# Optimization experiments

Hardware: AMD Instinct MI355X
Metric: run time of the kernel (lower is better)

The kernel has to match this reference:

```python
import jax, jax.numpy as jnp
import numpy as np
import math

N_HEADS = 32
N_KV_HEADS = 8
HEAD_DIM = 64
ROPE_BASE = 10000.0


def _rope_cos_sin(L, dtype):
    # inv_freq: [head_dim/2]
    inv_freq = 1.0 / (ROPE_BASE ** (jnp.arange(0, HEAD_DIM, 2, dtype=jnp.float32) / HEAD_DIM))
    t = jnp.arange(L, dtype=jnp.float32)
    freqs = jnp.outer(t, inv_freq)            # [L, head_dim/2]
    emb = jnp.concatenate([freqs, freqs], -1)  # [L, head_dim]
    return jnp.cos(emb).astype(dtype), jnp.sin(emb).astype(dtype)


def _rotate_half(x):
    x1, x2 = jnp.split(x, 2, axis=-1)
    return jnp.concatenate([-x2, x1], axis=-1)


def setup_inputs() -> dict:
    key = jax.random.key(0)
    ks = jax.random.split(key, 5)
    B, L, D = 2, 2048, 2048
    s = 0.02
    return {
        "x": jax.random.normal(ks[0], (B, L, D), jnp.float32),
        "Wq": jax.random.normal(ks[1], (D, N_HEADS * HEAD_DIM), jnp.float32) * s,
        "Wk": jax.random.normal(ks[2], (D, N_KV_HEADS * HEAD_DIM), jnp.float32) * s,
        "Wv": jax.random.normal(ks[3], (D, N_KV_HEADS * HEAD_DIM), jnp.float32) * s,
        "Wo": jax.random.normal(ks[4], (N_HEADS * HEAD_DIM, D), jnp.float32) * s,
    }


def reference(x, Wq, Wk, Wv, Wo):
    B, L, D = x.shape
    G = N_HEADS // N_KV_HEADS
    # QKV projections -> [B, H, L, hd]
    q = (x @ Wq).reshape(B, L, N_HEADS, HEAD_DIM).transpose(0, 2, 1, 3)
    k = (x @ Wk).reshape(B, L, N_KV_HEADS, HEAD_DIM).transpose(0, 2, 1, 3)
    v = (x @ Wv).reshape(B, L, N_KV_HEADS, HEAD_DIM).transpose(0, 2, 1, 3)
    # RoPE
    cos, sin = _rope_cos_sin(L, x.dtype)  # [L, hd]
    cos = cos[None, None]
    sin = sin[None, None]
    q = q * cos + _rotate_half(q) * sin
    k = k * cos + _rotate_half(k) * sin
    # GQA expand kv heads (repeat_interleave along head dim)
    k = jnp.repeat(k, G, axis=1)
    v = jnp.repeat(v, G, axis=1)
    # Causal SDPA
    scale = 1.0 / math.sqrt(HEAD_DIM)
    scores = jnp.einsum('bhqd,bhkd->bhqk', q, k) * scale  # [B,H,L,L]
    causal = jnp.tril(jnp.ones((L, L), bool))
    scores = jnp.where(causal[None, None], scores, jnp.finfo(scores.dtype).min)
    probs = jax.nn.softmax(scores, axis=-1)
    out = jnp.einsum('bhqk,bhkd->bhqd', probs, v)  # [B,H,L,hd]
    out = out.transpose(0, 2, 1, 3).reshape(B, L, N_HEADS * HEAD_DIM)
    return out @ Wo
```

## Files before the change

kernel.cpp:

```cpp
#include <hip/hip_runtime.h>
#include <hip/hip_bf16.h>
#include <stdint.h>

typedef __bf16 bf16_t;
typedef bf16_t bf16x2 __attribute__((ext_vector_type(2)));
typedef bf16_t bf16x4 __attribute__((ext_vector_type(4)));
typedef bf16_t bf16x8 __attribute__((ext_vector_type(8)));
typedef float f32x4 __attribute__((ext_vector_type(4)));
typedef float f32x16 __attribute__((ext_vector_type(16)));

#define NH 32
#define NKV 8
#define HD 64
#define LSEQ 2048
#define DMODEL 2048
#define BATCH 2

#define QSCALE 0.18033688011112042f
#define FIXED_M 12.0f

__device__ __forceinline__ void gl_lds16(const void* g, void* l) {
  __builtin_amdgcn_global_load_lds(
      (__attribute__((address_space(1))) char*)(uintptr_t)g,
      (__attribute__((address_space(3))) char*)(uintptr_t)l, 16, 0, 0);
}

__device__ __forceinline__ unsigned pack2(float a, float b) {
  bf16x2 t;
  t[0] = (bf16_t)a;
  t[1] = (bf16_t)b;
  return __builtin_bit_cast(unsigned, t);
}

__device__ __forceinline__ void transpose_tile32(
    const float* __restrict__ W, bf16_t* __restrict__ WT, int K, int N,
    int bi, float* tile ) {
  const int n32 = N >> 5;
  const int nb = (bi & (n32 - 1)) * 32, kb = (bi / n32) * 32;
  const int tx = threadIdx.x & 31, ty = threadIdx.x >> 5;
#pragma unroll
  for (int i = 0; i < 32; i += 8)
    tile[(ty + i) * 33 + tx] = W[(size_t)(kb + ty + i) * N + nb + tx];
  __syncthreads();
#pragma unroll
  for (int i = 0; i < 32; i += 8)
    WT[(size_t)(nb + ty + i) * K + kb + tx] = (bf16_t)tile[tx * 33 + ty + i];
}

__global__ __launch_bounds__(256) void prep_all(
    const float* __restrict__ x, const float* __restrict__ Wq,
    const float* __restrict__ Wk, const float* __restrict__ Wv,
    const float* __restrict__ Wo, bf16_t* __restrict__ xb,
    bf16_t* __restrict__ wqkvT, bf16_t* __restrict__ wot,
    float* __restrict__ cosT, float* __restrict__ sinT) {
  __shared__ float tile[32 * 33];
  const int bx = blockIdx.x;
  if (bx < 8192) {
    const int i = bx * 256 + threadIdx.x;
    const float4 v = ((const float4*)x)[i];
    bf16x4 o;
    o[0] = (bf16_t)v.x; o[1] = (bf16_t)v.y; o[2] = (bf16_t)v.z; o[3] = (bf16_t)v.w;
    ((bf16x4*)xb)[i] = o;
  } else if (bx < 12288) {
    transpose_tile32(Wq, wqkvT, 2048, 2048, bx - 8192, tile);
  } else if (bx < 13312) {
    transpose_tile32(Wk, wqkvT + (size_t)2048 * 2048, 2048, 512, bx - 12288, tile);
  } else if (bx < 14336) {
    transpose_tile32(Wv, wqkvT + (size_t)2560 * 2048, 2048, 512, bx - 13312, tile);
  } else if (bx < 18432) {
    transpose_tile32(Wo, wot, 2048, 2048, bx - 14336, tile);
  } else {
    const int t = (bx - 18432) * 256 + threadIdx.x;
    const int l = t >> 5, i = t & 31;
    const float inv = powf(10000.0f, -(float)i / 32.0f);
    const float ang = (float)l * inv;
    float s, c;
    sincosf(ang, &s, &c);
    cosT[t] = c;
    sinT[t] = s;
  }
}

template <int EPI>
__global__ __launch_bounds__(256, 3) void gemm128(
    const bf16_t* __restrict__ A, const bf16_t* __restrict__ BT,
    float* __restrict__ Cf, bf16_t* __restrict__ Qo, bf16_t* __restrict__ Ko,
    bf16_t* __restrict__ Vo, int M, int N, int K,
    const float* __restrict__ cosT, const float* __restrict__ sinT, int nx) {
  __shared__ bf16_t Al[128 * 64];
  __shared__ bf16_t Bl[128 * 64];
  const int tid = threadIdx.x, lane = tid & 63, w = tid >> 6;
  const int wm = w >> 1, wn = w & 1;
  const int r15 = lane & 15, g = lane >> 4;
  const int nwg = (int)gridDim.x;
  const int sid = ((int)blockIdx.x & 7) * (nwg >> 3) + ((int)blockIdx.x >> 3);
  const int m0 = (sid / nx) * 128, n0 = (sid % nx) * 128;
  f32x4 acc[4][4] = {};

  for (int kt = 0; kt < K; kt += 64) {
#pragma unroll
    for (int i = 0; i < 4; ++i) {
      const int c = i * 256 + tid;
      const int row = c >> 3, cc = c & 7;
      const int sc = (cc ^ (row & 7)) * 8;
      gl_lds16(A + (size_t)(m0 + row) * K + kt + sc, Al + c * 8);
      gl_lds16(BT + (size_t)(n0 + row) * K + kt + sc, Bl + c * 8);
    }
    __syncthreads();
#pragma unroll
    for (int kk = 0; kk < 2; ++kk) {
      bf16x8 af[4], bfr[4];
#pragma unroll
      for (int mi = 0; mi < 4; ++mi) {
        const int r = wm * 64 + mi * 16 + r15;
        af[mi] = *(const bf16x8*)((const char*)Al + r * 128 +
                                  (((kk * 4 + g) ^ (r & 7)) << 4));
      }
#pragma unroll
      for (int ni = 0; ni < 4; ++ni) {
        const int r = wn * 64 + ni * 16 + r15;
        bfr[ni] = *(const bf16x8*)((const char*)Bl + r * 128 +
                                   (((kk * 4 + g) ^ (r & 7)) << 4));
      }
#pragma unroll
      for (int mi = 0; mi < 4; ++mi)
#pragma unroll
        for (int ni = 0; ni < 4; ++ni)
          acc[mi][ni] = __builtin_amdgcn_mfma_f32_16x16x32_bf16(
              af[mi], bfr[ni], acc[mi][ni], 0, 0, 0);
    }
    __syncthreads();
  }

  if constexpr (EPI == 0) {
#pragma unroll
    for (int mi = 0; mi < 4; ++mi) {
      const int row = m0 + wm * 64 + mi * 16 + g * 4;
#pragma unroll
      for (int ni = 0; ni < 4; ++ni) {
        const int col = n0 + wn * 64 + ni * 16 + r15;
#pragma unroll
        for (int r = 0; r < 4; ++r)
          Cf[(size_t)(row + r) * N + col] = acc[mi][ni][r];
      }
    }
  } else {
    const int colbase = n0 + wn * 64;
    auto rope_store = [&](bf16_t* C, int NHT, int colrel, float sc) {
#pragma unroll
      for (int mi = 0; mi < 4; ++mi)
#pragma unroll
        for (int r = 0; r < 4; ++r) {
          const int rowg = m0 + wm * 64 + mi * 16 + g * 4 + r;
          const int bb = rowg >> 11, ls = rowg & (LSEQ - 1);
#pragma unroll
          for (int ni = 0; ni < 2; ++ni) {
            const int col = colrel + ni * 16 + r15;
            const int hh = col >> 6, d = col & 63;
            const float c = cosT[ls * 32 + d], s = sinT[ls * 32 + d];
            const float v0 = acc[mi][ni][r], v1 = acc[mi][ni + 2][r];
            bf16_t* dst = C + (((size_t)bb * NHT + hh) * LSEQ + ls) * HD + d;
            dst[0] = (bf16_t)((v0 * c - v1 * s) * sc);
            dst[32] = (bf16_t)((v1 * c + v0 * s) * sc);
          }
        }
    };
    if (n0 < 2048) {
      rope_store(Qo, NH, colbase, QSCALE);
    } else if (n0 < 2560) {
      rope_store(Ko, NKV, colbase - 2048, 1.0f);
    } else {
#pragma unroll
      for (int mi = 0; mi < 4; ++mi)
#pragma unroll
        for (int r = 0; r < 4; ++r) {
          const int rowg = m0 + wm * 64 + mi * 16 + g * 4 + r;
          const int bb = rowg >> 11, ls = rowg & (LSEQ - 1);
#pragma unroll
          for (int ni = 0; ni < 4; ++ni) {
            const int col = colbase - 2560 + ni * 16 + r15;
            const int hh = col >> 6, d = col & 63;
            Vo[(((size_t)bb * NKV + hh) * HD + d) * LSEQ + ls] =
                (bf16_t)acc[mi][ni][r];
          }
        }
    }
  }
}

template <int EPI, int NREP>
__global__ __launch_bounds__(512, 1) void gemm256(
    const bf16_t* __restrict__ A, const bf16_t* __restrict__ BT,
    float* __restrict__ Cf, int M, int N, int K, int nx) {
  __shared__ bf16_t Al[2][4 * 4096];
  __shared__ bf16_t Bl[2][NREP * 4096];
  const int tid = threadIdx.x, lane = tid & 63, w = tid >> 6;
  const int wm = w >> 2, wn = w & 3;
  const int r15 = lane & 15, g = lane >> 4;
  const int nwg = (int)gridDim.x;
  const int sid = ((int)blockIdx.x & 7) * (nwg >> 3) + ((int)blockIdx.x >> 3);
  const int m0 = (sid / nx) * 256, n0 = (sid % nx) * (NREP * 64);

  f32x4 acc[8][NREP] = {};

  const int NT = K >> 6;
  const int NI = NT >> 1;

  auto stage_q = [&](bf16_t* dst, const bf16_t* src, int row0, int kt) {
    const int r = tid >> 3;
    const int sc = (((tid & 7) ^ (r & 7)) << 3);
    gl_lds16(src + (size_t)(row0 + r) * K + (kt << 6) + sc, dst + tid * 8);
  };
  auto stage_step = [&](int d, int kt, int s) {
    kt = kt < NT ? kt : NT - 1;
    if (s == 0) { stage_q(&Bl[d][0], BT, n0, kt); stage_q(&Bl[d][4096], BT, n0 + 64, kt); }
    else if (s == 1) { stage_q(&Al[d][0], A, m0, kt); stage_q(&Al[d][8192], A, m0 + 128, kt); }
    else if (s == 2) { stage_q(&Al[d][4096], A, m0 + 64, kt); stage_q(&Al[d][12288], A, m0 + 192, kt); }
  };
  auto lda = [&](int d, int mi, int kk) -> bf16x8 {
    const int ar = (wm << 7) + (mi << 4) + r15;
    return *(const bf16x8*)((const char*)&Al[d][(ar >> 6) << 12] +
                            (ar & 63) * 128 + ((((kk << 2) + g) ^ (ar & 7)) << 4));
  };
  auto ldb = [&](int d, int ni, int kk) -> bf16x8 {
    const int br = wn * (NREP << 4) + (ni << 4) + r15;
    return *(const bf16x8*)((const char*)&Bl[d][(br >> 6) << 12] +
                            (br & 63) * 128 + ((((kk << 2) + g) ^ (br & 7)) << 4));
  };

  stage_step(0, 0, 0);
  stage_step(0, 0, 1);
  stage_step(0, 0, 2);
  stage_step(0, 0, 3);

  for (int i = 0; i < NI; ++i) {
#pragma unroll
    for (int hf = 0; hf < 2; ++hf) {
      const int dC = hf;
      const int dS = hf ^ 1;
      const int ktS = (i << 1) + 1 + hf;
      bf16x8 bf0[NREP][2];
#pragma unroll
      for (int q = 0; q < 4; ++q) {
        stage_step(dS, ktS, q);
        if (q == 0) asm volatile("s_waitcnt vmcnt(4)" ::: "memory");
        if (q == 2) asm volatile("s_waitcnt vmcnt(6)" ::: "memory");
        __builtin_amdgcn_s_barrier();
        asm volatile("" ::: "memory");
        if (q == 0) {
#pragma unroll
          for (int ni = 0; ni < NREP; ++ni)
#pragma unroll
            for (int kk = 0; kk < 2; ++kk) bf0[ni][kk] = ldb(dC, ni, kk);
        }
        bf16x8 af[2][2];
#pragma unroll
        for (int t2 = 0; t2 < 2; ++t2)
#pragma unroll
          for (int kk = 0; kk < 2; ++kk) af[t2][kk] = lda(dC, 2 * q + t2, kk);
        __builtin_amdgcn_s_setprio(1);
#pragma unroll
        for (int t2 = 0; t2 < 2; ++t2)
#pragma unroll
          for (int ni = 0; ni < NREP; ++ni)
#pragma unroll
            for (int kk = 0; kk < 2; ++kk)
              acc[2 * q + t2][ni] = __builtin_amdgcn_mfma_f32_16x16x32_bf16(
                  af[t2][kk], bf0[ni][kk], acc[2 * q + t2][ni], 0, 0, 0);
        __builtin_amdgcn_s_setprio(0);
        asm volatile("" ::: "memory");
        __builtin_amdgcn_s_barrier();
      }
    }
  }
  asm volatile("s_waitcnt vmcnt(0)" ::: "memory");

#pragma unroll
  for (int mi = 0; mi < 8; ++mi) {
    const int row = m0 + wm * 128 + mi * 16 + g * 4;
#pragma unroll
    for (int ni = 0; ni < NREP; ++ni) {
      const int col = n0 + wn * (NREP * 16) + ni * 16 + r15;
#pragma unroll
      for (int r = 0; r < 4; ++r)
        Cf[(size_t)(row + r) * N + col] = acc[mi][ni][r];
    }
  }
}

__global__ __launch_bounds__(512, 4) void attn_fwd(
    const bf16_t* __restrict__ Q, const bf16_t* __restrict__ Kh,
    const bf16_t* __restrict__ VTh, bf16_t* __restrict__ AO) {
  __shared__ bf16_t Kl[2][64 * 64];
  __shared__ bf16_t Vl[2][64 * 64];
  const int tid = threadIdx.x, lane = tid & 63, w = tid >> 6;
  const int col = lane & 31, hi = lane >> 5;
  const int hk = (int)blockIdx.x & 7, b = (int)blockIdx.x >> 3;
  const int a = (int)blockIdx.y & 15, k = (int)blockIdx.y >> 4;
  const int qt = k ? 31 - a : a;
  const int h = hk * 4 + (w & 3);
  const int qoff = (w >> 2) * 32;

  const bf16_t* Qb =
      Q + (((size_t)b * NH + h) * LSEQ + (size_t)qt * 64 + qoff) * HD;
  const bf16_t* Kb = Kh + ((size_t)b * NKV + hk) * LSEQ * HD;
  const bf16_t* Vb = VTh + ((size_t)b * NKV + hk) * HD * LSEQ;

  const int nt = qt + 1;

  bf16x8 ones8;
#pragma unroll
  for (int j = 0; j < 8; ++j) ones8[j] = (bf16_t)1.0f;

  auto stage = [&](int buf, int kt) {
    const int row = tid >> 3, cc = tid & 7;
    const int scol = (cc ^ (row & 7)) * 16;
    gl_lds16((const char*)Kb + (size_t)(kt * 64 + row) * 128 + scol,
             (char*)&Kl[buf][0] + tid * 16);
    gl_lds16((const char*)Vb + (size_t)row * 4096 + (size_t)kt * 128 + scol,
             (char*)&Vl[buf][0] + tid * 16);
  };

  bf16x8 qf[4];
#pragma unroll
  for (int kc = 0; kc < 4; ++kc)
    qf[kc] = *(const bf16x8*)&Qb[(size_t)col * HD + kc * 16 + hi * 8];

  f32x16 o[2] = {};
  f32x16 osum = {};

  int cur = 0;
  stage(cur, 0);
  __syncthreads();
  for (int kt = 0; kt < nt; ++kt) {
    if (kt + 1 < nt) stage(cur ^ 1, kt + 1);
    const bool diag = (kt == nt - 1);
    const char* Kcur = (const char*)&Kl[cur][0];
    const char* Vcur = (const char*)&Vl[cur][0];

    f32x16 sfrag[2] = {};
#pragma unroll
    for (int kvs = 0; kvs < 2; ++kvs) {
      if (diag && kvs * 32 > 31 + qoff) {
#pragma unroll
        for (int r = 0; r < 16; ++r) sfrag[kvs][r] = -1e30f;
        continue;
      }
      bf16x8 ak[4];
#pragma unroll
      for (int kc = 0; kc < 4; ++kc) {
        const int row = kvs * 32 + col;
        const int slot = ((kc * 2 + hi) ^ (row & 7)) * 16;
        ak[kc] = *(const bf16x8*)(Kcur + row * 128 + slot);
      }
#pragma unroll
      for (int kc = 0; kc < 4; ++kc)
        sfrag[kvs] = __builtin_amdgcn_mfma_f32_32x32x16_bf16(
            ak[kc], qf[kc], sfrag[kvs], 0, 0, 0);
    }

    if (diag) {
#pragma unroll
      for (int kvs = 0; kvs < 2; ++kvs)
#pragma unroll
        for (int r = 0; r < 16; ++r) {
          const int kvl = kvs * 32 + (r & 3) + 8 * (r >> 2) + 4 * hi;
          if (kvl > col + qoff) sfrag[kvs][r] = -1e30f;
        }
    }

    bf16x8 pf[4];
#pragma unroll
    for (int kvs = 0; kvs < 2; ++kvs)
#pragma unroll
      for (int c1 = 0; c1 < 2; ++c1) {
        float pv[8];
#pragma unroll
        for (int j = 0; j < 8; ++j)
          pv[j] = __builtin_amdgcn_exp2f(sfrag[kvs][c1 * 8 + j] - FIXED_M);
        const unsigned a01 = pack2(pv[0], pv[1]), a23 = pack2(pv[2], pv[3]);
        const unsigned b01 = pack2(pv[4], pv[5]), b23 = pack2(pv[6], pv[7]);
        const unsigned s01 = __shfl_xor(hi ? a01 : b01, 32);
        const unsigned s23 = __shfl_xor(hi ? a23 : b23, 32);
        union { unsigned u[4]; bf16x8 v; } t;
        t.u[0] = hi ? s01 : a01;
        t.u[1] = hi ? s23 : a23;
        t.u[2] = hi ? b01 : s01;
        t.u[3] = hi ? b23 : s23;
        pf[kvs * 2 + c1] = t.v;
      }

#pragma unroll
    for (int ds = 0; ds < 2; ++ds) {
      bf16x8 av[4];
#pragma unroll
      for (int kc2 = 0; kc2 < 4; ++kc2) {
        const int row = ds * 32 + col;
        const int slot = ((kc2 * 2 + hi) ^ (row & 7)) * 16;
        av[kc2] = *(const bf16x8*)(Vcur + row * 128 + slot);
      }
#pragma unroll
      for (int kc2 = 0; kc2 < 4; ++kc2) {
        if (diag && kc2 * 16 > 31 + qoff) continue;
        o[ds] = __builtin_amdgcn_mfma_f32_32x32x16_bf16(
            av[kc2], pf[kc2], o[ds], 0, 0, 0);
      }
    }
#pragma unroll
    for (int kc2 = 0; kc2 < 4; ++kc2) {
      if (diag && kc2 * 16 > 31 + qoff) continue;
      osum = __builtin_amdgcn_mfma_f32_32x32x16_bf16(
          ones8, pf[kc2], osum, 0, 0, 0);
    }

    __syncthreads();
    cur ^= 1;
  }

  const float inv = 1.0f / osum[0];
  const int q = qt * 64 + qoff + col;
#pragma unroll
  for (int ds = 0; ds < 2; ++ds)
#pragma unroll
    for (int g4 = 0; g4 < 4; ++g4) {
      bf16x4 o4;
#pragma unroll
      for (int j = 0; j < 4; ++j) o4[j] = (bf16_t)(o[ds][g4 * 4 + j] * inv);
      const int d = ds * 32 + 8 * g4 + 4 * hi;
      *(bf16x4*)&AO[((size_t)b * LSEQ + q) * DMODEL + h * HD + d] = o4;
    }
}


extern "C" void kernel_launch(void* const* d_in, const int* in_sizes, int n_in,
                              void* d_out, int out_size, void* d_ws, size_t ws_size,
                              hipStream_t stream) {
  const float* x = (const float*)d_in[0];
  const float* Wq = (const float*)d_in[1];
  const float* Wk = (const float*)d_in[2];
  const float* Wv = (const float*)d_in[3];
  const float* Wo = (const float*)d_in[4];
  char* ws = (char*)d_ws;
  size_t off = 0;
  auto alloc = [&](size_t bytes) {
    char* p = ws + off;
    off += (bytes + 255) & ~(size_t)255;
    return p;
  };
  bf16_t* xb = (bf16_t*)alloc((size_t)BATCH * LSEQ * DMODEL * 2);
  bf16_t* wqkvT = (bf16_t*)alloc((size_t)3072 * DMODEL * 2);
  bf16_t* wot = (bf16_t*)alloc((size_t)DMODEL * DMODEL * 2);
  float* cosT = (float*)alloc((size_t)LSEQ * 32 * 4);
  float* sinT = (float*)alloc((size_t)LSEQ * 32 * 4);
  bf16_t* Qh = (bf16_t*)alloc((size_t)BATCH * NH * LSEQ * HD * 2);
  bf16_t* Kh = (bf16_t*)alloc((size_t)BATCH * NKV * LSEQ * HD * 2);
  bf16_t* VTh = (bf16_t*)alloc((size_t)BATCH * NKV * HD * LSEQ * 2);
  bf16_t* AO = (bf16_t*)alloc((size_t)BATCH * LSEQ * NH * HD * 2);
  (void)ws_size; (void)in_sizes; (void)n_in; (void)out_size;

  const int M = BATCH * LSEQ;

  prep_all<<<18688, 256, 0, stream>>>(x, Wq, Wk, Wv, Wo, xb, wqkvT, wot,
                                      cosT, sinT);

  gemm128<3><<<768, 256, 0, stream>>>(
      xb, wqkvT, nullptr, Qh, Kh, VTh, M, 3072, 2048, cosT, sinT, 24);

  attn_fwd<<<dim3(16, 32), 512, 0, stream>>>(Qh, Kh, VTh, AO);

  gemm256<0, 2><<<256, 512, 0, stream>>>(
      AO, wot, (float*)d_out, M, 2048, 2048, 16);
}
```

Before: 164.8 us.

## Process two query sub-tiles per wave in attention and sum probabilities in registers

Attention blocks shrink from 8 to 4 waves. Each wave now handles all 64 query rows of its head, so every K/V fragment read from LDS is reused across two query halves. The ones-matrix MFMA that computed the softmax denominator is replaced by scalar register accumulation plus a cross-half shuffle. The trade-off is higher register pressure (two Q fragment sets, four O accumulators) and fewer waves per block to hide the staging latency.

New measurement: 175.7 us. 6.6% more time.

```diff
diff --git a/kernel.cpp b/kernel.cpp
--- a/kernel.cpp
+++ b/kernel.cpp
@@ -288,7 +288,7 @@
   }
 }
 
-__global__ __launch_bounds__(512, 4) void attn_fwd(
+__global__ __launch_bounds__(256, 2) void attn_fwd(
     const bf16_t* __restrict__ Q, const bf16_t* __restrict__ Kh,
     const bf16_t* __restrict__ VTh, bf16_t* __restrict__ AO) {
   __shared__ bf16_t Kl[2][64 * 64];
@@ -298,36 +298,37 @@
   const int hk = (int)blockIdx.x & 7, b = (int)blockIdx.x >> 3;
   const int a = (int)blockIdx.y & 15, k = (int)blockIdx.y >> 4;
   const int qt = k ? 31 - a : a;
-  const int h = hk * 4 + (w & 3);
-  const int qoff = (w >> 2) * 32;
-
-  const bf16_t* Qb =
-      Q + (((size_t)b * NH + h) * LSEQ + (size_t)qt * 64 + qoff) * HD;
+  const int h = hk * 4 + w;
+
+  const bf16_t* Qb = Q + (((size_t)b * NH + h) * LSEQ + (size_t)qt * 64) * HD;
   const bf16_t* Kb = Kh + ((size_t)b * NKV + hk) * LSEQ * HD;
   const bf16_t* Vb = VTh + ((size_t)b * NKV + hk) * HD * LSEQ;
 
   const int nt = qt + 1;
 
-  bf16x8 ones8;
-#pragma unroll
-  for (int j = 0; j < 8; ++j) ones8[j] = (bf16_t)1.0f;
-
   auto stage = [&](int buf, int kt) {
-    const int row = tid >> 3, cc = tid & 7;
-    const int scol = (cc ^ (row & 7)) * 16;
-    gl_lds16((const char*)Kb + (size_t)(kt * 64 + row) * 128 + scol,
-             (char*)&Kl[buf][0] + tid * 16);
-    gl_lds16((const char*)Vb + (size_t)row * 4096 + (size_t)kt * 128 + scol,
-             (char*)&Vl[buf][0] + tid * 16);
-  };
-
-  bf16x8 qf[4];
-#pragma unroll
-  for (int kc = 0; kc < 4; ++kc)
-    qf[kc] = *(const bf16x8*)&Qb[(size_t)col * HD + kc * 16 + hi * 8];
-
-  f32x16 o[2] = {};
-  f32x16 osum = {};
+#pragma unroll
+    for (int i = 0; i < 2; ++i) {
+      const int c = i * 256 + tid;
+      const int row = c >> 3, cc = c & 7;
+      const int scol = (cc ^ (row & 7)) * 16;
+      gl_lds16((const char*)Kb + (size_t)(kt * 64 + row) * 128 + scol,
+               (char*)&Kl[buf][0] + c * 16);
+      gl_lds16((const char*)Vb + (size_t)row * 4096 + (size_t)kt * 128 + scol,
+               (char*)&Vl[buf][0] + c * 16);
+    }
+  };
+
+  bf16x8 qf[2][4];
+#pragma unroll
+  for (int qh = 0; qh < 2; ++qh)
+#pragma unroll
+    for (int kc = 0; kc < 4; ++kc)
+      qf[qh][kc] =
+          *(const bf16x8*)&Qb[(size_t)(qh * 32 + col) * HD + kc * 16 + hi * 8];
+
+  f32x16 o[2][2] = {};
+  float lsum[2] = {0.f, 0.f};
 
   int cur = 0;
   stage(cur, 0);
@@ -338,14 +339,9 @@
     const char* Kcur = (const char*)&Kl[cur][0];
     const char* Vcur = (const char*)&Vl[cur][0];
 
-    f32x16 sfrag[2] = {};
+    bf16x8 pf[2][4];
 #pragma unroll
     for (int kvs = 0; kvs < 2; ++kvs) {
-      if (diag && kvs * 32 > 31 + qoff) {
-#pragma unroll
-        for (int r = 0; r < 16; ++r) sfrag[kvs][r] = -1e30f;
-        continue;
-      }
       bf16x8 ak[4];
 #pragma unroll
       for (int kc = 0; kc < 4; ++kc) {
@@ -354,41 +350,41 @@
         ak[kc] = *(const bf16x8*)(Kcur + row * 128 + slot);
       }
 #pragma unroll
-      for (int kc = 0; kc < 4; ++kc)
-        sfrag[kvs] = __builtin_amdgcn_mfma_f32_32x32x16_bf16(
-            ak[kc], qf[kc], sfrag[kvs], 0, 0, 0);
-    }
-
-    if (diag) {
-#pragma unroll
-      for (int kvs = 0; kvs < 2; ++kvs)
-#pragma unroll
-        for (int r = 0; r < 16; ++r) {
-          const int kvl = kvs * 32 + (r & 3) + 8 * (r >> 2) + 4 * hi;
-          if (kvl > col + qoff) sfrag[kvs][r] = -1e30f;
-        }
-    }
-
-    bf16x8 pf[4];
-#pragma unroll
-    for (int kvs = 0; kvs < 2; ++kvs)
-#pragma unroll
-      for (int c1 = 0; c1 < 2; ++c1) {
-        float pv[8];
-#pragma unroll
-        for (int j = 0; j < 8; ++j)
-          pv[j] = __builtin_amdgcn_exp2f(sfrag[kvs][c1 * 8 + j] - FIXED_M);
-        const unsigned a01 = pack2(pv[0], pv[1]), a23 = pack2(pv[2], pv[3]);
-        const unsigned b01 = pack2(pv[4], pv[5]), b23 = pack2(pv[6], pv[7]);
-        const unsigned s01 = __shfl_xor(hi ? a01 : b01, 32);
-        const unsigned s23 = __shfl_xor(hi ? a23 : b23, 32);
-        union { unsigned u[4]; bf16x8 v; } t;
-        t.u[0] = hi ? s01 : a01;
-        t.u[1] = hi ? s23 : a23;
-        t.u[2] = hi ? b01 : s01;
-        t.u[3] = hi ? b23 : s23;
-        pf[kvs * 2 + c1] = t.v;
-      }
+      for (int qh = 0; qh < 2; ++qh) {
+        if (diag && kvs == 1 && qh == 0) continue;
+        f32x16 sf = {};
+#pragma unroll
+        for (int kc = 0; kc < 4; ++kc)
+          sf = __builtin_amdgcn_mfma_f32_32x32x16_bf16(ak[kc], qf[qh][kc], sf,
+                                                       0, 0, 0);
+        if (diag && kvs == qh) {
+#pragma unroll
+          for (int r = 0; r < 16; ++r) {
+            const int kvl = (r & 3) + 8 * (r >> 2) + 4 * hi;
+            if (kvl > col) sf[r] = -1e30f;
+          }
+        }
+#pragma unroll
+        for (int c1 = 0; c1 < 2; ++c1) {
+          float pv[8];
+#pragma unroll
+          for (int j = 0; j < 8; ++j) {
+            pv[j] = __builtin_amdgcn_exp2f(sf[c1 * 8 + j] - FIXED_M);
+            lsum[qh] += pv[j];
+          }
+          const unsigned a01 = pack2(pv[0], pv[1]), a23 = pack2(pv[2], pv[3]);
+          const unsigned b01 = pack2(pv[4], pv[5]), b23 = pack2(pv[6], pv[7]);
+          const unsigned s01 = __shfl_xor(hi ? a01 : b01, 32);
+          const unsigned s23 = __shfl_xor(hi ? a23 : b23, 32);
+          union { unsigned u[4]; bf16x8 v; } t;
+          t.u[0] = hi ? s01 : a01;
+          t.u[1] = hi ? s23 : a23;
+          t.u[2] = hi ? b01 : s01;
+          t.u[3] = hi ? b23 : s23;
+          pf[qh][kvs * 2 + c1] = t.v;
+        }
+      }
+    }
 
 #pragma unroll
     for (int ds = 0; ds < 2; ++ds) {
@@ -400,35 +396,36 @@
         av[kc2] = *(const bf16x8*)(Vcur + row * 128 + slot);
       }
 #pragma unroll
-      for (int kc2 = 0; kc2 < 4; ++kc2) {
-        if (diag && kc2 * 16 > 31 + qoff) continue;
-        o[ds] = __builtin_amdgcn_mfma_f32_32x32x16_bf16(
-            av[kc2], pf[kc2], o[ds], 0, 0, 0);
-      }
-    }
-#pragma unroll
-    for (int kc2 = 0; kc2 < 4; ++kc2) {
-      if (diag && kc2 * 16 > 31 + qoff) continue;
-      osum = __builtin_amdgcn_mfma_f32_32x32x16_bf16(
-          ones8, pf[kc2], osum, 0, 0, 0);
+      for (int qh = 0; qh < 2; ++qh)
+#pragma unroll
+        for (int kc2 = 0; kc2 < 4; ++kc2) {
+          if (diag && qh == 0 && kc2 >= 2) continue;
+          o[ds][qh] = __builtin_amdgcn_mfma_f32_32x32x16_bf16(
+              av[kc2], pf[qh][kc2], o[ds][qh], 0, 0, 0);
+        }
     }
 
     __syncthreads();
     cur ^= 1;
   }
 
-  const float inv = 1.0f / osum[0];
-  const int q = qt * 64 + qoff + col;
-#pragma unroll
-  for (int ds = 0; ds < 2; ++ds)
-#pragma unroll
-    for (int g4 = 0; g4 < 4; ++g4) {
-      bf16x4 o4;
-#pragma unroll
-      for (int j = 0; j < 4; ++j) o4[j] = (bf16_t)(o[ds][g4 * 4 + j] * inv);
-      const int d = ds * 32 + 8 * g4 + 4 * hi;
-      *(bf16x4*)&AO[((size_t)b * LSEQ + q) * DMODEL + h * HD + d] = o4;
-    }
+#pragma unroll
+  for (int qh = 0; qh < 2; ++qh) {
+    float l = lsum[qh] + __shfl_xor(lsum[qh], 32);
+    const float inv = 1.0f / l;
+    const int q = qt * 64 + qh * 32 + col;
+#pragma unroll
+    for (int ds = 0; ds < 2; ++ds)
+#pragma unroll
+      for (int g4 = 0; g4 < 4; ++g4) {
+        bf16x4 o4;
+#pragma unroll
+        for (int j = 0; j < 4; ++j)
+          o4[j] = (bf16_t)(o[ds][qh][g4 * 4 + j] * inv);
+        const int d = ds * 32 + 8 * g4 + 4 * hi;
+        *(bf16x4*)&AO[((size_t)b * LSEQ + q) * DMODEL + h * HD + d] = o4;
+      }
+  }
 }
 
 
@@ -466,7 +463,7 @@
   gemm128<3><<<768, 256, 0, stream>>>(
       xb, wqkvT, nullptr, Qh, Kh, VTh, M, 3072, 2048, cosT, sinT, 24);
 
-  attn_fwd<<<dim3(16, 32), 512, 0, stream>>>(Qh, Kh, VTh, AO);
+  attn_fwd<<<dim3(16, 32), 256, 0, stream>>>(Qh, Kh, VTh, AO);
 
   gemm256<0, 2><<<256, 512, 0, stream>>>(
       AO, wot, (float*)d_out, M, 2048, 2048, 16);
```
